# Performance work log

Hardware: AMD Instinct MI355X
Metric: run time of the kernel (lower is better)

Reference implementation:

```python
import jax, jax.numpy as jnp
import numpy as np

N_NODES = 50000
N_EDGES = 800000
D_FEAT = 64


def setup_inputs() -> dict:
    key = jax.random.key(0)
    k1, k2, k3 = jax.random.split(key, 3)
    xs = jax.random.normal(k1, (N_NODES, D_FEAT), dtype=jnp.float32)
    src = jax.random.randint(k2, (N_EDGES,), 0, N_NODES, dtype=jnp.int32)
    dst = jax.random.randint(k3, (N_EDGES,), 0, N_NODES, dtype=jnp.int32)
    return {"xs": xs, "src": src, "dst": dst}


def reference(xs, src, dst):
    # Edge-list scatter-mean: for each edge (src=ee, dst=i), accumulate
    # xs[ee] into bucket i, then divide by the bucket count.
    gathered = xs[src]                                   # [E, D]
    sums = jax.ops.segment_sum(gathered, dst, num_segments=N_NODES)  # [N, D]
    counts = jax.ops.segment_sum(
        jnp.ones((src.shape[0],), dtype=xs.dtype), dst, num_segments=N_NODES
    )                                                    # [N]
    # Original only emits groups that appear; here empty groups yield 0.
    return sums / jnp.maximum(counts, 1.0)[:, None]
```

## Files before the change

### kernel.cpp

```cpp
#include <hip/hip_runtime.h>

#define N_NODES 50000
#define N_EDGES 800000
#define D_FEAT 64

#define NPART 200
#define EPP (N_EDGES / NPART)
#define NBINS_F ((N_NODES + 63) / 64)
#define LCAP 4096

__global__ __launch_bounds__(1024) void part_hist_kernel(const int* __restrict__ dst,
                                                         int* __restrict__ histBB) {
    __shared__ int h[NBINS_F];
    int t = threadIdx.x, blk = blockIdx.x;
    if (t < NBINS_F) h[t] = 0;
    __syncthreads();
    int base = blk * EPP;
    for (int i = t; i < EPP; i += 1024)
        atomicAdd(&h[dst[base + i] >> 6], 1);
    __syncthreads();
    if (t < NBINS_F) histBB[blk * NBINS_F + t] = h[t];
}

__global__ void col_scan_kernel(const int* __restrict__ histBB,
                                int* __restrict__ baseBB,
                                int* __restrict__ binTot) {
    __shared__ int lds[256];
    int bin = blockIdx.x, t = threadIdx.x;
    int v = (t < NPART) ? histBB[t * NBINS_F + bin] : 0;
    lds[t] = v;
    __syncthreads();
    for (int off = 1; off < 256; off <<= 1) {
        int x = (t >= off) ? lds[t - off] : 0;
        __syncthreads();
        lds[t] += x;
        __syncthreads();
    }
    if (t < NPART) baseBB[t * NBINS_F + bin] = lds[t] - v;
    if (t == 255) binTot[bin] = lds[255];
}

__global__ __launch_bounds__(1024) void bin_scan_kernel(const int* __restrict__ binTot,
                                                        int* __restrict__ binBase) {
    __shared__ int wsum[16];
    int t = threadIdx.x;
    int v = (t < NBINS_F) ? binTot[t] : 0;
    int lane = t & 63, wave = t >> 6;
    int incl = v;
    #pragma unroll
    for (int o = 1; o < 64; o <<= 1) { int x = __shfl_up(incl, o); if (lane >= o) incl += x; }
    if (lane == 63) wsum[wave] = incl;
    __syncthreads();
    int wbase = 0;
    #pragma unroll
    for (int w = 0; w < 16; ++w) wbase += (w < wave) ? wsum[w] : 0;
    if (t < NBINS_F) binBase[t] = wbase + incl - v;
    if (t == NBINS_F - 1) binBase[NBINS_F] = wbase + incl;
}

__global__ __launch_bounds__(1024) void part_scatter_kernel(const int* __restrict__ src,
                                                            const int* __restrict__ dst,
                                                            const int* __restrict__ baseBB,
                                                            const int* __restrict__ binBase,
                                                            unsigned int* __restrict__ staging) {
    __shared__ int cur[NBINS_F];
    int t = threadIdx.x, blk = blockIdx.x;
    if (t < NBINS_F) cur[t] = binBase[t] + baseBB[blk * NBINS_F + t];
    __syncthreads();
    int base = blk * EPP;
    for (int i = t; i < EPP; i += 1024) {
        int d = dst[base + i];
        int bin = d >> 6;
        int pos = atomicAdd(&cur[bin], 1);
        staging[pos] = (unsigned int)src[base + i] | ((unsigned int)(d & 63) << 16);
    }
}

__global__ __launch_bounds__(256) void sort_to_csr_kernel(const unsigned int* __restrict__ staging,
                                                          const int* __restrict__ binBase,
                                                          unsigned short* __restrict__ esorted,
                                                          int* __restrict__ offs) {
    __shared__ int cntL[64];
    __shared__ int off[65];
    __shared__ int cur[64];
    __shared__ unsigned short list[LCAP];
    int bin = blockIdx.x, t = threadIdx.x;
    int lo = binBase[bin], hi = binBase[bin + 1];
    int n = hi - lo;
    int nodeLo = bin << 6;

    if (t < 64) cntL[t] = 0;
    __syncthreads();
    for (int i = lo + t; i < hi; i += 256)
        atomicAdd(&cntL[(staging[i] >> 16) & 63], 1);
    __syncthreads();
    if (t < 64) {
        int v = cntL[t];
        int incl = v;
        #pragma unroll
        for (int o = 1; o < 64; o <<= 1) { int x = __shfl_up(incl, o); if (t >= o) incl += x; }
        off[t] = incl - v;
        cur[t] = incl - v;
    }
    __syncthreads();
    if (t < 64) {
        int node = nodeLo + t;
        if (node < N_NODES) offs[node] = lo + off[t];
    }
    if (bin == NBINS_F - 1 && t == 0) offs[N_NODES] = N_EDGES;

    if (n <= LCAP) {
        for (int i = lo + t; i < hi; i += 256) {
            unsigned int pk = staging[i];
            int p = atomicAdd(&cur[(pk >> 16) & 63], 1);
            list[p] = (unsigned short)pk;
        }
        __syncthreads();
        for (int i = t; i < n; i += 256)
            esorted[lo + i] = list[i];
    } else {
        for (int i = lo + t; i < hi; i += 256) {
            unsigned int pk = staging[i];
            int p = atomicAdd(&cur[(pk >> 16) & 63], 1);
            esorted[lo + p] = (unsigned short)pk;
        }
    }
}

__global__ __launch_bounds__(256) void csr_pull_kernel(const float* __restrict__ xs,
                                                       const unsigned short* __restrict__ esorted,
                                                       const int* __restrict__ offs,
                                                       float* __restrict__ out) {
    int tid = blockIdx.x * 256 + threadIdx.x;
    int node = tid >> 4;
    int c = tid & 15;
    int beg = offs[node];
    int end = offs[node + 1];
    int deg = end - beg;
    float4 acc = make_float4(0.f, 0.f, 0.f, 0.f);
    for (int j0 = 0; j0 < deg; j0 += 16) {
        int rem = deg - j0;
        int m = rem < 16 ? rem : 16;
        int myid = (c < m) ? (int)__builtin_nontemporal_load(esorted + beg + j0 + c) : 0;
        if (m == 16) {
            #pragma unroll
            for (int k = 0; k < 16; ++k) {
                int s = __shfl(myid, k, 16);
                const float4 v = *reinterpret_cast<const float4*>(xs + s * D_FEAT + c * 4);
                acc.x += v.x; acc.y += v.y; acc.z += v.z; acc.w += v.w;
            }
        } else {
            for (int k = 0; k < m; ++k) {
                int s = __shfl(myid, k, 16);
                const float4 v = *reinterpret_cast<const float4*>(xs + s * D_FEAT + c * 4);
                acc.x += v.x; acc.y += v.y; acc.z += v.z; acc.w += v.w;
            }
        }
    }
    float inv = 1.0f / fmaxf((float)deg, 1.0f);
    float* op = out + (size_t)node * D_FEAT + c * 4;
    __builtin_nontemporal_store(acc.x * inv, op + 0);
    __builtin_nontemporal_store(acc.y * inv, op + 1);
    __builtin_nontemporal_store(acc.z * inv, op + 2);
    __builtin_nontemporal_store(acc.w * inv, op + 3);
}


__global__ void scatter_kernel(const float* __restrict__ xs,
                               const int* __restrict__ src,
                               const int* __restrict__ dst,
                               float* __restrict__ sums,
                               float* __restrict__ counts) {
    int tid = blockIdx.x * blockDim.x + threadIdx.x;
    int e = tid >> 4;
    int c = tid & 15;
    if (e >= N_EDGES) return;
    int s = src[e];
    int d = dst[e];
    const float4 v = *reinterpret_cast<const float4*>(xs + (size_t)s * D_FEAT + c * 4);
    float* outp = sums + (size_t)d * D_FEAT + c * 4;
    atomicAdd(outp + 0, v.x);
    atomicAdd(outp + 1, v.y);
    atomicAdd(outp + 2, v.z);
    atomicAdd(outp + 3, v.w);
    if (c == 0) atomicAdd(counts + d, 1.0f);
}

__global__ void divide_kernel(float* __restrict__ out, const float* __restrict__ counts) {
    int tid = blockIdx.x * blockDim.x + threadIdx.x;
    if (tid >= N_NODES * D_FEAT / 4) return;
    int node = tid >> 4;
    float inv = 1.0f / fmaxf(counts[node], 1.0f);
    float4 v = reinterpret_cast<const float4*>(out)[tid];
    v.x *= inv; v.y *= inv; v.z *= inv; v.w *= inv;
    reinterpret_cast<float4*>(out)[tid] = v;
}


extern "C" void kernel_launch(void* const* d_in, const int* in_sizes, int n_in,
                              void* d_out, int out_size, void* d_ws, size_t ws_size,
                              hipStream_t stream) {
    const float* xs  = (const float*)d_in[0];
    const int*   src = (const int*)d_in[1];
    const int*   dst = (const int*)d_in[2];
    float* out = (float*)d_out;

    size_t need = (size_t)(2 * NPART * NBINS_F + NBINS_F + (NBINS_F + 1) + (N_NODES + 1)) * sizeof(int)
                + (size_t)N_EDGES * sizeof(unsigned int)
                + (size_t)N_EDGES * sizeof(unsigned short);
    if (ws_size < need) {
        float* counts = (float*)d_ws;
        hipMemsetAsync(out, 0, (size_t)N_NODES * D_FEAT * sizeof(float), stream);
        hipMemsetAsync(counts, 0, (size_t)N_NODES * sizeof(float), stream);
        scatter_kernel<<<(N_EDGES * 16 + 255) / 256, 256, 0, stream>>>(xs, src, dst, out, counts);
        divide_kernel<<<(N_NODES * D_FEAT / 4 + 255) / 256, 256, 0, stream>>>(out, counts);
        return;
    }

    int* ws = (int*)d_ws;
    int* histBB  = ws;
    int* baseBB  = histBB + NPART * NBINS_F;
    int* binTot  = baseBB + NPART * NBINS_F;
    int* binBase = binTot + NBINS_F;
    int* offs    = binBase + NBINS_F + 1;
    unsigned int* staging = (unsigned int*)(offs + N_NODES + 1);
    unsigned short* esorted = (unsigned short*)(staging + N_EDGES);

    part_hist_kernel<<<NPART, 1024, 0, stream>>>(dst, histBB);
    col_scan_kernel<<<NBINS_F, 256, 0, stream>>>(histBB, baseBB, binTot);
    bin_scan_kernel<<<1, 1024, 0, stream>>>(binTot, binBase);
    part_scatter_kernel<<<NPART, 1024, 0, stream>>>(src, dst, baseBB, binBase, staging);
    sort_to_csr_kernel<<<NBINS_F, 256, 0, stream>>>(staging, binBase, esorted, offs);
    csr_pull_kernel<<<(N_NODES * 16) / 256, 256, 0, stream>>>(xs, esorted, offs, out);
}
```

Measured before the change: 124.2 us.

## Coarsen radix partition to 512-node buckets with block-level local sort

Widens the first-pass partition from 64-node bins (782 bins) to 512-node buckets (98 buckets). Histogram, column scan and scatter work shrinks, and fewer, more contiguous staging runs are written. The local sort now uses 512-thread blocks with a multi-wave scan and a 12K-entry LDS list. The risk is that only 98 blocks fill the GPU for the sort stage, which may reduce parallelism there.

Result: no change. 124.4 us (+0.2%).

```diff
diff --git a/kernel.cpp b/kernel.cpp
--- a/kernel.cpp
+++ b/kernel.cpp
@@ -6,20 +6,22 @@
 
 #define NPART 200
 #define EPP (N_EDGES / NPART)
-#define NBINS_F ((N_NODES + 63) / 64)
-#define LCAP 4096
+#define BIG_SHIFT 9
+#define BIG_NODES 512
+#define NBIG ((N_NODES + BIG_NODES - 1) / BIG_NODES)
+#define SCAP 12288
 
 __global__ __launch_bounds__(1024) void part_hist_kernel(const int* __restrict__ dst,
                                                          int* __restrict__ histBB) {
-    __shared__ int h[NBINS_F];
+    __shared__ int h[NBIG];
     int t = threadIdx.x, blk = blockIdx.x;
-    if (t < NBINS_F) h[t] = 0;
+    if (t < NBIG) h[t] = 0;
     __syncthreads();
     int base = blk * EPP;
     for (int i = t; i < EPP; i += 1024)
-        atomicAdd(&h[dst[base + i] >> 6], 1);
-    __syncthreads();
-    if (t < NBINS_F) histBB[blk * NBINS_F + t] = h[t];
+        atomicAdd(&h[dst[base + i] >> BIG_SHIFT], 1);
+    __syncthreads();
+    if (t < NBIG) histBB[blk * NBIG + t] = h[t];
 }
 
 __global__ void col_scan_kernel(const int* __restrict__ histBB,
@@ -27,7 +29,7 @@
                                 int* __restrict__ binTot) {
     __shared__ int lds[256];
     int bin = blockIdx.x, t = threadIdx.x;
-    int v = (t < NPART) ? histBB[t * NBINS_F + bin] : 0;
+    int v = (t < NPART) ? histBB[t * NBIG + bin] : 0;
     lds[t] = v;
     __syncthreads();
     for (int off = 1; off < 256; off <<= 1) {
@@ -36,26 +38,23 @@
         lds[t] += x;
         __syncthreads();
     }
-    if (t < NPART) baseBB[t * NBINS_F + bin] = lds[t] - v;
+    if (t < NPART) baseBB[t * NBIG + bin] = lds[t] - v;
     if (t == 255) binTot[bin] = lds[255];
 }
 
-__global__ __launch_bounds__(1024) void bin_scan_kernel(const int* __restrict__ binTot,
-                                                        int* __restrict__ binBase) {
-    __shared__ int wsum[16];
+__global__ void bin_scan_kernel(const int* __restrict__ binTot, int* __restrict__ binBase) {
+    __shared__ int wsum[2];
     int t = threadIdx.x;
-    int v = (t < NBINS_F) ? binTot[t] : 0;
+    int v = (t < NBIG) ? binTot[t] : 0;
     int lane = t & 63, wave = t >> 6;
     int incl = v;
     #pragma unroll
     for (int o = 1; o < 64; o <<= 1) { int x = __shfl_up(incl, o); if (lane >= o) incl += x; }
     if (lane == 63) wsum[wave] = incl;
     __syncthreads();
-    int wbase = 0;
-    #pragma unroll
-    for (int w = 0; w < 16; ++w) wbase += (w < wave) ? wsum[w] : 0;
-    if (t < NBINS_F) binBase[t] = wbase + incl - v;
-    if (t == NBINS_F - 1) binBase[NBINS_F] = wbase + incl;
+    int base = (wave == 1) ? wsum[0] : 0;
+    if (t < NBIG) binBase[t] = base + incl - v;
+    if (t == NBIG - 1) binBase[NBIG] = base + incl;
 }
 
 __global__ __launch_bounds__(1024) void part_scatter_kernel(const int* __restrict__ src,
@@ -63,65 +62,70 @@
                                                             const int* __restrict__ baseBB,
                                                             const int* __restrict__ binBase,
                                                             unsigned int* __restrict__ staging) {
-    __shared__ int cur[NBINS_F];
+    __shared__ int cur[NBIG];
     int t = threadIdx.x, blk = blockIdx.x;
-    if (t < NBINS_F) cur[t] = binBase[t] + baseBB[blk * NBINS_F + t];
+    if (t < NBIG) cur[t] = binBase[t] + baseBB[blk * NBIG + t];
     __syncthreads();
     int base = blk * EPP;
     for (int i = t; i < EPP; i += 1024) {
         int d = dst[base + i];
-        int bin = d >> 6;
+        int bin = d >> BIG_SHIFT;
         int pos = atomicAdd(&cur[bin], 1);
-        staging[pos] = (unsigned int)src[base + i] | ((unsigned int)(d & 63) << 16);
-    }
-}
-
-__global__ __launch_bounds__(256) void sort_to_csr_kernel(const unsigned int* __restrict__ staging,
-                                                          const int* __restrict__ binBase,
-                                                          unsigned short* __restrict__ esorted,
-                                                          int* __restrict__ offs) {
-    __shared__ int cntL[64];
-    __shared__ int off[65];
-    __shared__ int cur[64];
-    __shared__ unsigned short list[LCAP];
+        staging[pos] = (unsigned int)src[base + i] |
+                       ((unsigned int)(d & (BIG_NODES - 1)) << 16);
+    }
+}
+
+__global__ __launch_bounds__(512) void sort512_kernel(const unsigned int* __restrict__ staging,
+                                                      const int* __restrict__ binBase,
+                                                      unsigned short* __restrict__ esorted,
+                                                      int* __restrict__ offs) {
+    __shared__ int cnt[BIG_NODES];
+    __shared__ int cur[BIG_NODES];
+    __shared__ unsigned short list[SCAP];
+    __shared__ int wsum[8];
     int bin = blockIdx.x, t = threadIdx.x;
     int lo = binBase[bin], hi = binBase[bin + 1];
     int n = hi - lo;
-    int nodeLo = bin << 6;
-
-    if (t < 64) cntL[t] = 0;
-    __syncthreads();
-    for (int i = lo + t; i < hi; i += 256)
-        atomicAdd(&cntL[(staging[i] >> 16) & 63], 1);
-    __syncthreads();
-    if (t < 64) {
-        int v = cntL[t];
-        int incl = v;
-        #pragma unroll
-        for (int o = 1; o < 64; o <<= 1) { int x = __shfl_up(incl, o); if (t >= o) incl += x; }
-        off[t] = incl - v;
-        cur[t] = incl - v;
-    }
-    __syncthreads();
-    if (t < 64) {
-        int node = nodeLo + t;
-        if (node < N_NODES) offs[node] = lo + off[t];
-    }
-    if (bin == NBINS_F - 1 && t == 0) offs[N_NODES] = N_EDGES;
-
-    if (n <= LCAP) {
-        for (int i = lo + t; i < hi; i += 256) {
+    int nodeLo = bin << BIG_SHIFT;
+
+    cnt[t] = 0;
+    __syncthreads();
+    for (int i = lo + t; i < hi; i += 512)
+        atomicAdd(&cnt[(staging[i] >> 16) & (BIG_NODES - 1)], 1);
+    __syncthreads();
+
+    int v = cnt[t];
+    int lane = t & 63, wave = t >> 6;
+    int incl = v;
+    #pragma unroll
+    for (int o = 1; o < 64; o <<= 1) { int x = __shfl_up(incl, o); if (lane >= o) incl += x; }
+    if (lane == 63) wsum[wave] = incl;
+    __syncthreads();
+    int wbase = 0;
+    #pragma unroll
+    for (int w = 0; w < 8; ++w) wbase += (w < wave) ? wsum[w] : 0;
+    int excl = wbase + incl - v;
+    cur[t] = excl;
+
+    int node = nodeLo + t;
+    if (node < N_NODES) offs[node] = lo + excl;
+    if (bin == NBIG - 1 && t == 0) offs[N_NODES] = N_EDGES;
+    __syncthreads();
+
+    if (n <= SCAP) {
+        for (int i = lo + t; i < hi; i += 512) {
             unsigned int pk = staging[i];
-            int p = atomicAdd(&cur[(pk >> 16) & 63], 1);
+            int p = atomicAdd(&cur[(pk >> 16) & (BIG_NODES - 1)], 1);
             list[p] = (unsigned short)pk;
         }
         __syncthreads();
-        for (int i = t; i < n; i += 256)
+        for (int i = t; i < n; i += 512)
             esorted[lo + i] = list[i];
     } else {
-        for (int i = lo + t; i < hi; i += 256) {
+        for (int i = lo + t; i < hi; i += 512) {
             unsigned int pk = staging[i];
-            int p = atomicAdd(&cur[(pk >> 16) & 63], 1);
+            int p = atomicAdd(&cur[(pk >> 16) & (BIG_NODES - 1)], 1);
             esorted[lo + p] = (unsigned short)pk;
         }
     }
@@ -205,7 +209,7 @@
     const int*   dst = (const int*)d_in[2];
     float* out = (float*)d_out;
 
-    size_t need = (size_t)(2 * NPART * NBINS_F + NBINS_F + (NBINS_F + 1) + (N_NODES + 1)) * sizeof(int)
+    size_t need = (size_t)(2 * NPART * NBIG + NBIG + (NBIG + 1) + (N_NODES + 1)) * sizeof(int)
                 + (size_t)N_EDGES * sizeof(unsigned int)
                 + (size_t)N_EDGES * sizeof(unsigned short);
     if (ws_size < need) {
@@ -219,17 +223,17 @@
 
     int* ws = (int*)d_ws;
     int* histBB  = ws;
-    int* baseBB  = histBB + NPART * NBINS_F;
-    int* binTot  = baseBB + NPART * NBINS_F;
-    int* binBase = binTot + NBINS_F;
-    int* offs    = binBase + NBINS_F + 1;
+    int* baseBB  = histBB + NPART * NBIG;
+    int* binTot  = baseBB + NPART * NBIG;
+    int* binBase = binTot + NBIG;
+    int* offs    = binBase + NBIG + 1;
     unsigned int* staging = (unsigned int*)(offs + N_NODES + 1);
     unsigned short* esorted = (unsigned short*)(staging + N_EDGES);
 
     part_hist_kernel<<<NPART, 1024, 0, stream>>>(dst, histBB);
-    col_scan_kernel<<<NBINS_F, 256, 0, stream>>>(histBB, baseBB, binTot);
-    bin_scan_kernel<<<1, 1024, 0, stream>>>(binTot, binBase);
+    col_scan_kernel<<<NBIG, 256, 0, stream>>>(histBB, baseBB, binTot);
+    bin_scan_kernel<<<1, 128, 0, stream>>>(binTot, binBase);
     part_scatter_kernel<<<NPART, 1024, 0, stream>>>(src, dst, baseBB, binBase, staging);
-    sort_to_csr_kernel<<<NBINS_F, 256, 0, stream>>>(staging, binBase, esorted, offs);
+    sort512_kernel<<<NBIG, 512, 0, stream>>>(staging, binBase, esorted, offs);
     csr_pull_kernel<<<(N_NODES * 16) / 256, 256, 0, stream>>>(xs, esorted, offs, out);
 }
```
